# Kernel tuning notes

Hardware: AMD Instinct MI355X
Metric: run time of the kernel (lower is better)

The kernel has to match this reference:

```python
import jax, jax.numpy as jnp
import numpy as np

B, T, INPUT, HIDDEN, NQ = 256, 512, 128, 128, 4


def rx_mat(theta):
    # RX(theta) = [[cos(t/2), -i sin(t/2)], [-i sin(t/2), cos(t/2)]]
    th = theta * 0.5
    c = jnp.cos(th).astype(jnp.complex64)
    s = (-1j) * jnp.sin(th).astype(jnp.complex64)
    return jnp.stack([jnp.stack([c, s], -1), jnp.stack([s, c], -1)], -2)


def cnot(s, ctrl, tgt):
    # statevector s: (B, 2,2,2,2); qubit w lives on axis w+1
    a0 = jax.lax.index_in_dim(s, 0, ctrl + 1, keepdims=True)
    a1 = jax.lax.index_in_dim(s, 1, ctrl + 1, keepdims=True)
    a1 = jnp.flip(a1, axis=tgt + 1)  # X on target when control=1
    return jnp.concatenate([a0, a1], axis=ctrl + 1)


def run_circuit(y, theta):
    # y: (B, 4) encoder angles (data), theta: (4,) trainable RX angles
    b = y.shape[0]
    s = jnp.zeros((b, 2, 2, 2, 2), jnp.complex64).at[:, 0, 0, 0, 0].set(1.0)
    Ue = rx_mat(y)      # (B, 4, 2, 2)
    s = jnp.einsum('bpA,bABCD->bpBCD', Ue[:, 0], s)
    s = jnp.einsum('bpB,bABCD->bApCD', Ue[:, 1], s)
    s = jnp.einsum('bpC,bABCD->bABpD', Ue[:, 2], s)
    s = jnp.einsum('bpD,bABCD->bABCp', Ue[:, 3], s)
    Ut = rx_mat(theta)  # (4, 2, 2)
    s = jnp.einsum('pA,bABCD->bpBCD', Ut[0], s)
    s = jnp.einsum('pB,bABCD->bApCD', Ut[1], s)
    s = jnp.einsum('pC,bABCD->bABpD', Ut[2], s)
    s = jnp.einsum('pD,bABCD->bABCp', Ut[3], s)
    for c_w, t_w in ((0, 1), (1, 2), (2, 3), (3, 0)):  # ring CNOTs
        s = cnot(s, c_w, t_w)
    probs = s.real ** 2 + s.imag ** 2
    z = jnp.array([1.0, -1.0], jnp.float32)
    return jnp.stack([
        jnp.einsum('bABCD,A->b', probs, z),
        jnp.einsum('bABCD,B->b', probs, z),
        jnp.einsum('bABCD,C->b', probs, z),
        jnp.einsum('bABCD,D->b', probs, z)], axis=-1)  # (B, 4) <Z_w>


def setup_inputs() -> dict:
    key = jax.random.key(0)
    ks = jax.random.split(key, 6)
    x = jax.random.normal(ks[0], (B, T, INPUT), jnp.float32)
    W_in = jax.random.normal(ks[1], (NQ, INPUT + HIDDEN), jnp.float32) / np.float32(np.sqrt(INPUT + HIDDEN))
    b_in = jax.random.normal(ks[2], (NQ,), jnp.float32) * 0.01
    W_out = jax.random.normal(ks[3], (HIDDEN, NQ), jnp.float32) * 0.5
    b_out = jax.random.normal(ks[4], (HIDDEN,), jnp.float32) * 0.01
    thetas = jax.random.uniform(ks[5], (4, NQ), jnp.float32, 0.0, 2.0 * np.pi)
    return {"x": x, "W_in": W_in, "b_in": b_in, "W_out": W_out, "b_out": b_out, "thetas": thetas}


def reference(x, W_in, b_in, W_out, b_out, thetas):
    bsz = x.shape[0]
    h0 = jnp.zeros((bsz, HIDDEN), x.dtype)
    c0 = jnp.zeros((bsz, HIDDEN), x.dtype)
    circuits = jax.vmap(run_circuit, in_axes=(None, 0))  # over 4 gate layers

    def step(carry, x_t):
        h, c = carry
        v = jnp.concatenate([h, x_t], axis=1)           # (B, H+I)
        y = v @ W_in.T + b_in                           # (B, 4)
        m = circuits(y, thetas)                         # (4, B, 4)
        proj = jnp.einsum('gbq,hq->gbh', m, W_out) + b_out  # shared clayer_out
        f = jax.nn.sigmoid(proj[0])
        i = jax.nn.sigmoid(proj[1])
        g = jnp.tanh(proj[2])
        o = jax.nn.sigmoid(proj[3])
        c = f * c + i * g
        h = o * jnp.tanh(c)
        return (h, c), h

    (h_t, c_t), hs = jax.lax.scan(step, (h0, c0), jnp.swapaxes(x, 0, 1))
    hidden_seq = jnp.swapaxes(hs, 0, 1)  # (B, T, H)
    return hidden_seq, h_t, c_t
```

## Files before the change

kernel.cpp:

```cpp
#include <hip/hip_runtime.h>

#define BATCH  256
#define TLEN   512
#define NIN    128
#define NHID   128

#define INV2PI 0.15915494309189535f
#define NL2E  -1.4426950408889634f
#define N2L2E -2.8853900817779268f

__device__ __forceinline__ float wave_sum_bcast(float x) {
    int v = __float_as_int(x);
#define RSTEP(ctrl)                                                          \
    { int t_ = __builtin_amdgcn_update_dpp(0, v, (ctrl), 0xf, 0xf, true);    \
      v = __float_as_int(__int_as_float(v) + __int_as_float(t_)); }
    RSTEP(0x111)
    RSTEP(0x112)
    RSTEP(0x114)
    RSTEP(0x118)
    RSTEP(0x142)
    RSTEP(0x143)
#undef RSTEP
    return __int_as_float(__builtin_amdgcn_readlane(v, 63));
}

__global__ __launch_bounds__(256) void y_pre_kernel(
    const float* __restrict__ x, const float* __restrict__ W_in,
    const float* __restrict__ b_in, float* __restrict__ out)
{
    const int lane = threadIdx.x & 63;
    const int wv   = threadIdx.x >> 6;
    const int bt   = (blockIdx.x << 2) + wv;

    const float xa = x[(size_t)bt * NIN + lane];
    const float xb = x[(size_t)bt * NIN + 64 + lane];

    float yq[4];
#pragma unroll
    for (int q = 0; q < 4; ++q) {
        const float p = xa * W_in[q * 256 + 128 + lane]
                      + xb * W_in[q * 256 + 192 + lane];
        yq[q] = (wave_sum_bcast(p) + b_in[q]) * INV2PI;
    }
    if (lane < 4) {
        const float v = (lane == 0) ? yq[0] : (lane == 1) ? yq[1]
                      : (lane == 2) ? yq[2] : yq[3];
        out[(size_t)bt * NHID + lane] = v;
    }
}

__global__ __launch_bounds__(256, 1) void qlstm_rec_kernel(
    const float* __restrict__ W_in,
    const float* __restrict__ thetas,
    const float* __restrict__ W_out,
    const float* __restrict__ b_out,
    float* __restrict__ out)
{
    const int b    = blockIdx.x;
    const int lane = threadIdx.x & 63;
    const int wv   = threadIdx.x >> 6;

    __shared__ float h_sh[128];
    __shared__ __align__(16) float cs_sh[16];

    const float whA = W_in[wv * 256 + lane]      * INV2PI;
    const float whB = W_in[wv * 256 + 64 + lane] * INV2PI;
    float th2[4];
#pragma unroll
    for (int g = 0; g < 4; ++g) th2[g] = thetas[g * 4 + wv] * INV2PI;

    const int hidx = wv * 32 + (lane & 31);
    const float gsc[4] = {NL2E, NL2E, N2L2E, NL2E};
    float wos[4][4], bos[4];
#pragma unroll
    for (int g = 0; g < 4; ++g) {
        bos[g] = gsc[g] * b_out[hidx];
#pragma unroll
        for (int q = 0; q < 4; ++q) wos[g][q] = gsc[g] * W_out[hidx * 4 + q];
    }

    float c = 0.0f, h_st = 0.0f;
    if (threadIdx.x < 128) h_sh[threadIdx.x] = 0.0f;
    __syncthreads();

    float* orow = out + (size_t)b * TLEN * NHID;

    float Yp[4];
#pragma unroll
    for (int d = 0; d < 4; ++d) Yp[d] = orow[d * NHID + wv];

    for (int tb = 0; tb < TLEN; tb += 4) {
#pragma unroll
        for (int d = 0; d < 4; ++d) {
            const int t = tb + d;

            if (t > 0) orow[(t - 1) * NHID + hidx] = h_st;
            const float Ysc = Yp[d];
            const int   tn  = (t + 4 < TLEN) ? t + 4 : TLEN - 1;
            Yp[d] = orow[tn * NHID + wv];

            const float ha = h_sh[lane];
            const float hb = h_sh[64 + lane];
            const float y  = wave_sum_bcast(ha * whA + hb * whB);
            float cg0 = __builtin_amdgcn_cosf(y + (Ysc + th2[0]));
            float cg1 = __builtin_amdgcn_cosf(y + (Ysc + th2[1]));
            float cg2 = __builtin_amdgcn_cosf(y + (Ysc + th2[2]));
            float cg3 = __builtin_amdgcn_cosf(y + (Ysc + th2[3]));
            if (lane == 0)
                *(float4*)&cs_sh[wv * 4] = make_float4(cg0, cg1, cg2, cg3);
            __syncthreads();

            const float4 q0 = *(const float4*)&cs_sh[0];
            const float4 q1 = *(const float4*)&cs_sh[4];
            const float4 q2 = *(const float4*)&cs_sh[8];
            const float4 q3 = *(const float4*)&cs_sh[12];

            float pr[4];
#define GATE(G, C0, C1, C2, C3)                                              \
            {                                                                \
                const float a_  = (C1) * (C2);                               \
                const float m0_ = a_ * (C3);                                 \
                const float m1_ = (C0) * (C1);                               \
                const float m2_ = (C0) * a_;                                 \
                const float m3_ = m2_ * (C3);                                \
                pr[G] = bos[G] + m0_ * wos[G][0] + m1_ * wos[G][1]           \
                               + m2_ * wos[G][2] + m3_ * wos[G][3];          \
            }
            GATE(0, q0.x, q1.x, q2.x, q3.x)
            GATE(1, q0.y, q1.y, q2.y, q3.y)
            GATE(2, q0.z, q1.z, q2.z, q3.z)
            GATE(3, q0.w, q1.w, q2.w, q3.w)
#undef GATE

            const float ef = __builtin_amdgcn_exp2f(pr[0]);
            const float ei = __builtin_amdgcn_exp2f(pr[1]);
            const float eg = __builtin_amdgcn_exp2f(pr[2]);
            const float eo = __builtin_amdgcn_exp2f(pr[3]);
            const float f  = __builtin_amdgcn_rcpf(1.0f + ef);
            const float i  = __builtin_amdgcn_rcpf(1.0f + ei);
            const float sg = __builtin_amdgcn_rcpf(1.0f + eg);
            const float o  = __builtin_amdgcn_rcpf(1.0f + eo);
            const float g2 = __builtin_fmaf(2.0f, sg, -1.0f);
            c = f * c + i * g2;
            const float ec = __builtin_amdgcn_exp2f(c * N2L2E);
            const float st = __builtin_amdgcn_rcpf(1.0f + ec);
            const float h  = o * __builtin_fmaf(2.0f, st, -1.0f);

            h_st = h;
            h_sh[hidx] = h;
            __syncthreads();
        }
    }

    orow[(TLEN - 1) * NHID + hidx] = h_st;
    float* ht = out + (size_t)BATCH * TLEN * NHID;
    float* ct = ht + (size_t)BATCH * NHID;
    ht[b * NHID + hidx] = h_st;
    ct[b * NHID + hidx] = c;
}

extern "C" void kernel_launch(void* const* d_in, const int* in_sizes, int n_in,
                              void* d_out, int out_size, void* d_ws, size_t ws_size,
                              hipStream_t stream) {
    const float* x      = (const float*)d_in[0];
    const float* W_in   = (const float*)d_in[1];
    const float* b_in   = (const float*)d_in[2];
    const float* W_out  = (const float*)d_in[3];
    const float* b_out  = (const float*)d_in[4];
    const float* thetas = (const float*)d_in[5];
    float* out = (float*)d_out;

    y_pre_kernel<<<dim3((BATCH * TLEN) / 4), dim3(256), 0, stream>>>(
        x, W_in, b_in, out);

    qlstm_rec_kernel<<<dim3(BATCH), dim3(256), 0, stream>>>(
        W_in, thetas, W_out, b_out, out);
}
```

Baseline: 334.9 us.

## Replicate hidden-state update in every wave to drop one barrier per step

Each of the four waves now redundantly computes all 128 hidden/cell values, two per lane, so h no longer goes through shared memory and the second block barrier per timestep is removed. The cosine exchange buffer is double-buffered so a single barrier per step suffices, and a custom barrier waits only on LDS counters rather than also on global memory operations. This trades four-fold redundant gate arithmetic for fewer synchronisations on the serial recurrence critical path.

```diff
diff --git a/kernel.cpp b/kernel.cpp
--- a/kernel.cpp
+++ b/kernel.cpp
@@ -22,6 +22,10 @@
     RSTEP(0x143)
 #undef RSTEP
     return __int_as_float(__builtin_amdgcn_readlane(v, 63));
+}
+
+__device__ __forceinline__ void barrier_lds() {
+    asm volatile("s_waitcnt lgkmcnt(0)\n\ts_barrier" ::: "memory");
 }
 
 __global__ __launch_bounds__(256) void y_pre_kernel(
@@ -60,8 +64,7 @@
     const int lane = threadIdx.x & 63;
     const int wv   = threadIdx.x >> 6;
 
-    __shared__ float h_sh[128];
-    __shared__ __align__(16) float cs_sh[16];
+    __shared__ __align__(16) float cs_sh[2][16];
 
     const float whA = W_in[wv * 256 + lane]      * INV2PI;
     const float whB = W_in[wv * 256 + 64 + lane] * INV2PI;
@@ -69,20 +72,20 @@
 #pragma unroll
     for (int g = 0; g < 4; ++g) th2[g] = thetas[g * 4 + wv] * INV2PI;
 
-    const int hidx = wv * 32 + (lane & 31);
     const float gsc[4] = {NL2E, NL2E, N2L2E, NL2E};
-    float wos[4][4], bos[4];
+    float wos0[4][4], wos1[4][4], bos0[4], bos1[4];
 #pragma unroll
     for (int g = 0; g < 4; ++g) {
-        bos[g] = gsc[g] * b_out[hidx];
+        bos0[g] = gsc[g] * b_out[lane];
+        bos1[g] = gsc[g] * b_out[64 + lane];
 #pragma unroll
-        for (int q = 0; q < 4; ++q) wos[g][q] = gsc[g] * W_out[hidx * 4 + q];
+        for (int q = 0; q < 4; ++q) {
+            wos0[g][q] = gsc[g] * W_out[lane * 4 + q];
+            wos1[g][q] = gsc[g] * W_out[(64 + lane) * 4 + q];
+        }
     }
 
-    float c = 0.0f, h_st = 0.0f;
-    if (threadIdx.x < 128) h_sh[threadIdx.x] = 0.0f;
-    __syncthreads();
-
+    float h0 = 0.0f, h1 = 0.0f, c0 = 0.0f, c1 = 0.0f;
     float* orow = out + (size_t)b * TLEN * NHID;
 
     float Yp[4];
@@ -94,28 +97,31 @@
         for (int d = 0; d < 4; ++d) {
             const int t = tb + d;
 
-            if (t > 0) orow[(t - 1) * NHID + hidx] = h_st;
-            const float Ysc = Yp[d];
-            const int   tn  = (t + 4 < TLEN) ? t + 4 : TLEN - 1;
+            if (t > 0) {
+                if (wv == 0)      orow[(t - 1) * NHID + lane]      = h0;
+                else if (wv == 1) orow[(t - 1) * NHID + 64 + lane] = h1;
+            }
+
+            const float p    = h0 * whA + h1 * whB;
+            const float base = wave_sum_bcast(p) + Yp[d];
+            const float cg0 = __builtin_amdgcn_cosf(base + th2[0]);
+            const float cg1 = __builtin_amdgcn_cosf(base + th2[1]);
+            const float cg2 = __builtin_amdgcn_cosf(base + th2[2]);
+            const float cg3 = __builtin_amdgcn_cosf(base + th2[3]);
+            if (lane == 0)
+                *(float4*)&cs_sh[d & 1][wv * 4] = make_float4(cg0, cg1, cg2, cg3);
+
+            const int tn = (t + 4 < TLEN) ? t + 4 : TLEN - 1;
             Yp[d] = orow[tn * NHID + wv];
 
-            const float ha = h_sh[lane];
-            const float hb = h_sh[64 + lane];
-            const float y  = wave_sum_bcast(ha * whA + hb * whB);
-            float cg0 = __builtin_amdgcn_cosf(y + (Ysc + th2[0]));
-            float cg1 = __builtin_amdgcn_cosf(y + (Ysc + th2[1]));
-            float cg2 = __builtin_amdgcn_cosf(y + (Ysc + th2[2]));
-            float cg3 = __builtin_amdgcn_cosf(y + (Ysc + th2[3]));
-            if (lane == 0)
-                *(float4*)&cs_sh[wv * 4] = make_float4(cg0, cg1, cg2, cg3);
-            __syncthreads();
+            barrier_lds();
 
-            const float4 q0 = *(const float4*)&cs_sh[0];
-            const float4 q1 = *(const float4*)&cs_sh[4];
-            const float4 q2 = *(const float4*)&cs_sh[8];
-            const float4 q3 = *(const float4*)&cs_sh[12];
+            const float4 q0 = *(const float4*)&cs_sh[d & 1][0];
+            const float4 q1 = *(const float4*)&cs_sh[d & 1][4];
+            const float4 q2 = *(const float4*)&cs_sh[d & 1][8];
+            const float4 q3 = *(const float4*)&cs_sh[d & 1][12];
 
-            float pr[4];
+            float pr0[4], pr1[4];
 #define GATE(G, C0, C1, C2, C3)                                              \
             {                                                                \
                 const float a_  = (C1) * (C2);                               \
@@ -123,8 +129,10 @@
                 const float m1_ = (C0) * (C1);                               \
                 const float m2_ = (C0) * a_;                                 \
                 const float m3_ = m2_ * (C3);                                \
-                pr[G] = bos[G] + m0_ * wos[G][0] + m1_ * wos[G][1]           \
-                               + m2_ * wos[G][2] + m3_ * wos[G][3];          \
+                pr0[G] = bos0[G] + m0_ * wos0[G][0] + m1_ * wos0[G][1]       \
+                                 + m2_ * wos0[G][2] + m3_ * wos0[G][3];      \
+                pr1[G] = bos1[G] + m0_ * wos1[G][0] + m1_ * wos1[G][1]       \
+                                 + m2_ * wos1[G][2] + m3_ * wos1[G][3];      \
             }
             GATE(0, q0.x, q1.x, q2.x, q3.x)
             GATE(1, q0.y, q1.y, q2.y, q3.y)
@@ -132,31 +140,40 @@
             GATE(3, q0.w, q1.w, q2.w, q3.w)
 #undef GATE
 
-            const float ef = __builtin_amdgcn_exp2f(pr[0]);
-            const float ei = __builtin_amdgcn_exp2f(pr[1]);
-            const float eg = __builtin_amdgcn_exp2f(pr[2]);
-            const float eo = __builtin_amdgcn_exp2f(pr[3]);
-            const float f  = __builtin_amdgcn_rcpf(1.0f + ef);
-            const float i  = __builtin_amdgcn_rcpf(1.0f + ei);
-            const float sg = __builtin_amdgcn_rcpf(1.0f + eg);
-            const float o  = __builtin_amdgcn_rcpf(1.0f + eo);
-            const float g2 = __builtin_fmaf(2.0f, sg, -1.0f);
-            c = f * c + i * g2;
-            const float ec = __builtin_amdgcn_exp2f(c * N2L2E);
-            const float st = __builtin_amdgcn_rcpf(1.0f + ec);
-            const float h  = o * __builtin_fmaf(2.0f, st, -1.0f);
-
-            h_st = h;
-            h_sh[hidx] = h;
-            __syncthreads();
+            {
+                const float f  = __builtin_amdgcn_rcpf(1.0f + __builtin_amdgcn_exp2f(pr0[0]));
+                const float i  = __builtin_amdgcn_rcpf(1.0f + __builtin_amdgcn_exp2f(pr0[1]));
+                const float sg = __builtin_amdgcn_rcpf(1.0f + __builtin_amdgcn_exp2f(pr0[2]));
+                const float o  = __builtin_amdgcn_rcpf(1.0f + __builtin_amdgcn_exp2f(pr0[3]));
+                const float g2 = __builtin_fmaf(2.0f, sg, -1.0f);
+                c0 = f * c0 + i * g2;
+                const float st = __builtin_amdgcn_rcpf(1.0f + __builtin_amdgcn_exp2f(c0 * N2L2E));
+                h0 = o * __builtin_fmaf(2.0f, st, -1.0f);
+            }
+            {
+                const float f  = __builtin_amdgcn_rcpf(1.0f + __builtin_amdgcn_exp2f(pr1[0]));
+                const float i  = __builtin_amdgcn_rcpf(1.0f + __builtin_amdgcn_exp2f(pr1[1]));
+                const float sg = __builtin_amdgcn_rcpf(1.0f + __builtin_amdgcn_exp2f(pr1[2]));
+                const float o  = __builtin_amdgcn_rcpf(1.0f + __builtin_amdgcn_exp2f(pr1[3]));
+                const float g2 = __builtin_fmaf(2.0f, sg, -1.0f);
+                c1 = f * c1 + i * g2;
+                const float st = __builtin_amdgcn_rcpf(1.0f + __builtin_amdgcn_exp2f(c1 * N2L2E));
+                h1 = o * __builtin_fmaf(2.0f, st, -1.0f);
+            }
         }
     }
 
-    orow[(TLEN - 1) * NHID + hidx] = h_st;
     float* ht = out + (size_t)BATCH * TLEN * NHID;
     float* ct = ht + (size_t)BATCH * NHID;
-    ht[b * NHID + hidx] = h_st;
-    ct[b * NHID + hidx] = c;
+    if (wv == 0) {
+        orow[(TLEN - 1) * NHID + lane] = h0;
+        ht[b * NHID + lane] = h0;
+        ct[b * NHID + lane] = c0;
+    } else if (wv == 1) {
+        orow[(TLEN - 1) * NHID + 64 + lane] = h1;
+        ht[b * NHID + 64 + lane] = h1;
+        ct[b * NHID + 64 + lane] = c1;
+    }
 }
 
 extern "C" void kernel_launch(void* const* d_in, const int* in_sizes, int n_in,
```

Measured after the change: 332.7 us. About the same (-0.7%).
